# Kernel optimization log

Measured on AMD Instinct MI355X. Metric: run time of the kernel, lower is better.

The kernel has to match this reference:

```python
import jax, jax.numpy as jnp
import numpy as np

V, E, H, L = 32000, 512, 512, 2   # vocab, emb_dim, hidden_dim, lstm layers
IN = 2 * H                        # input_size (= enc_output feature dim)
B, S_ENC, T_DEC = 32, 128, 64


def setup_inputs() -> dict:
    key = jax.random.key(0)
    ks = jax.random.split(key, 20)
    sc = 0.05
    inp = {
        "tokens": jax.random.randint(ks[0], (B, T_DEC), 0, V),
        "enc_output": jax.random.normal(ks[1], (B, S_ENC, IN), jnp.float32),
        "enc_h": jax.random.normal(ks[2], (L, B, H), jnp.float32),
        "enc_c": jax.random.normal(ks[3], (L, B, H), jnp.float32),
        "emb": jax.random.normal(ks[4], (V, E), jnp.float32) * sc,
        # attention MLP: attn1 in = H*L + IN, out = 4H; attn2: 4H -> 1
        "attn1_w": jax.random.normal(ks[5], (4 * H, H * L + IN), jnp.float32) * sc,
        "attn1_b": jnp.zeros((4 * H,), jnp.float32),
        "attn2_w": jax.random.normal(ks[6], (1, 4 * H), jnp.float32) * sc,
        "attn2_b": jnp.zeros((1,), jnp.float32),
        # LSTM layer 0: input E + IN; layer 1: input H. PyTorch gate order i,f,g,o
        "w_ih0": jax.random.normal(ks[7], (4 * H, E + IN), jnp.float32) * sc,
        "w_hh0": jax.random.normal(ks[8], (4 * H, H), jnp.float32) * sc,
        "b_ih0": jnp.zeros((4 * H,), jnp.float32),
        "b_hh0": jnp.zeros((4 * H,), jnp.float32),
        "w_ih1": jax.random.normal(ks[9], (4 * H, H), jnp.float32) * sc,
        "w_hh1": jax.random.normal(ks[10], (4 * H, H), jnp.float32) * sc,
        "b_ih1": jnp.zeros((4 * H,), jnp.float32),
        "b_hh1": jnp.zeros((4 * H,), jnp.float32),
        "out_w": jax.random.normal(ks[11], (V, H), jnp.float32) * sc,
        "out_b": jnp.zeros((V,), jnp.float32),
    }
    return inp


def _lstm_cell(x, h, c, w_ih, w_hh, b_ih, b_hh):
    g = x @ w_ih.T + h @ w_hh.T + (b_ih + b_hh)
    i, f, gg, o = jnp.split(g, 4, axis=-1)
    c_new = jax.nn.sigmoid(f) * c + jax.nn.sigmoid(i) * jnp.tanh(gg)
    h_new = jax.nn.sigmoid(o) * jnp.tanh(c_new)
    return h_new, c_new


def reference(tokens, enc_output, enc_h, enc_c, emb,
              attn1_w, attn1_b, attn2_w, attn2_b,
              w_ih0, w_hh0, b_ih0, b_hh0,
              w_ih1, w_hh1, b_ih1, b_hh1,
              out_w, out_b):
    b, s_enc = enc_output.shape[0], enc_output.shape[1]

    def context(h):  # h: [L, B, H] -> context: [B, 2H]
        hflat = jnp.transpose(h, (1, 0, 2)).reshape(b, -1)          # [B, L*H]
        hexp = jnp.broadcast_to(hflat[:, None, :], (b, s_enc, hflat.shape[-1]))
        ai = jnp.concatenate([enc_output, hexp], axis=-1)           # [B, S, 2H+L*H]
        hid = ai @ attn1_w.T + attn1_b                               # [B, S, 4H]
        logits = hid @ attn2_w.T + attn2_b                           # [B, S, 1]
        w = jax.nn.softmax(logits, axis=1)
        return jnp.sum(enc_output * w, axis=1)                       # [B, 2H]

    def step(carry, emb_t):  # emb_t: [B, E]
        h, c = carry
        ctx = context(h)
        x = jnp.concatenate([emb_t, ctx], axis=-1)                   # [B, E+2H]
        h0, c0 = _lstm_cell(x, h[0], c[0], w_ih0, w_hh0, b_ih0, b_hh0)
        h1, c1 = _lstm_cell(h0, h[1], c[1], w_ih1, w_hh1, b_ih1, b_hh1)
        return (jnp.stack([h0, h1]), jnp.stack([c0, c1])), h1

    emb_seq = jnp.transpose(emb[tokens], (1, 0, 2))                  # [T, B, E]
    _, outs = jax.lax.scan(step, (enc_h, enc_c), emb_seq)            # [T, B, H]
    dec = jnp.transpose(outs, (1, 0, 2))                             # [B, T, H]
    return dec @ out_w.T + out_b                                     # [B, T, V]
```

## Files before the change

kernel.cpp:

```cpp
#include <hip/hip_runtime.h>
#include <hip/hip_bf16.h>

typedef __attribute__((ext_vector_type(4))) float f4v;
typedef __attribute__((ext_vector_type(4))) short s4v;
typedef __attribute__((ext_vector_type(8))) short s8v;

#define DEVINL __device__ __forceinline__
#define NBLK 128
#define PADK 536
#define WROWS (16 * PADK)
#define HSLOT 16384

DEVINL short f2bf(float f) {
  unsigned u = __float_as_uint(f);
  u += 0x7FFFu + ((u >> 16) & 1u);
  return (short)(u >> 16);
}
DEVINL float bf2f(short s) {
  return __uint_as_float(((unsigned)(unsigned short)s) << 16);
}
DEVINL float sigm(float x) { return 1.f / (1.f + expf(-x)); }

DEVINL void cstore64(short* p, unsigned long long d) {
  asm volatile("global_store_dwordx2 %0, %1, off sc0 sc1"
               :: "v"(p), "v"(d) : "memory");
}

__global__ __launch_bounds__(256) void k_init2(const float* __restrict__ enc_h,
                                               short* __restrict__ hbuf,
                                               unsigned* __restrict__ arr) {
  int i = blockIdx.x * 256 + threadIdx.x;
  hbuf[i] = f2bf(enc_h[i]);
  hbuf[(long)65 * HSLOT + i] = f2bf(enc_h[16384 + i]);
  if (i < NBLK * 32 + 32) arr[i] = 0u;
}

__global__ __launch_bounds__(256) void k_weff(const float* __restrict__ attn1_w,
                                              const float* __restrict__ attn2_w,
                                              float* __restrict__ w_enc) {
  __shared__ float part[8][32];
  int t = threadIdx.x;
  int jl = t & 31, kp = t >> 5;
  int j = blockIdx.x * 32 + jl;
  float acc = 0.f;
  for (int k = kp * 256; k < kp * 256 + 256; ++k)
    acc += attn2_w[k] * attn1_w[(long)k * 2048 + j];
  part[kp][jl] = acc;
  __syncthreads();
  if (t < 32) {
    float s = 0.f;
    for (int p = 0; p < 8; ++p) s += part[p][t];
    w_enc[blockIdx.x * 32 + t] = s;
  }
}

__global__ __launch_bounds__(256) void k_attn(const float* __restrict__ enc,
                                              const float* __restrict__ w_enc,
                                              float* __restrict__ ctx) {
  __shared__ float red[256];
  __shared__ float wls[128];
  int b = blockIdx.x, t = threadIdx.x;
  int s = t >> 1, half = t & 1;
  const float* e = enc + ((long)b * 128 + s) * 1024 + half * 512;
  const float* wv = w_enc + half * 512;
  float acc = 0.f;
  for (int k = 0; k < 512; k += 4) {
    f4v ev = *(const f4v*)(e + k);
    f4v w4 = *(const f4v*)(wv + k);
    acc += ev[0] * w4[0] + ev[1] * w4[1] + ev[2] * w4[2] + ev[3] * w4[3];
  }
  red[t] = acc;
  __syncthreads();
  if (half == 0) wls[s] = red[t] + red[t + 1];
  __syncthreads();
  red[t] = (t < 128) ? wls[t] : -3.4e38f;
  __syncthreads();
  for (int off = 128; off >= 1; off >>= 1) {
    if (t < off) red[t] = fmaxf(red[t], red[t + off]);
    __syncthreads();
  }
  float mx = red[0];
  __syncthreads();
  if (t < 128) { float ex = expf(wls[t] - mx); wls[t] = ex; red[t] = ex; }
  else red[t] = 0.f;
  __syncthreads();
  for (int off = 128; off >= 1; off >>= 1) {
    if (t < off) red[t] += red[t + off];
    __syncthreads();
  }
  float inv = 1.f / red[0];
  __syncthreads();
  if (t < 128) wls[t] *= inv;
  __syncthreads();
  float a0 = 0.f, a1 = 0.f, a2 = 0.f, a3 = 0.f;
  for (int ss = 0; ss < 128; ++ss) {
    float w = wls[ss];
    const float* er = enc + ((long)b * 128 + ss) * 1024;
    a0 += w * er[t];
    a1 += w * er[t + 256];
    a2 += w * er[t + 512];
    a3 += w * er[t + 768];
  }
  ctx[b * 1024 + t] = a0;
  ctx[b * 1024 + t + 256] = a1;
  ctx[b * 1024 + t + 512] = a2;
  ctx[b * 1024 + t + 768] = a3;
}

__global__ __launch_bounds__(256) void k_ctxpre(const float* __restrict__ w_ih0,
                                                const float* __restrict__ b_ih0,
                                                const float* __restrict__ b_hh0,
                                                const float* __restrict__ ctx,
                                                float* __restrict__ ctxpre) {
  int t = threadIdx.x;
  int j = blockIdx.x * 8 + (t >> 5);
  int b = t & 31;
  float acc = b_ih0[j] + b_hh0[j];
  const float* w = w_ih0 + (long)j * 1536 + 512;
  const float* c = ctx + b * 1024;
  for (int k = 0; k < 1024; k += 4) {
    f4v wv = *(const f4v*)(w + k);
    f4v cv = *(const f4v*)(c + k);
    acc += wv[0] * cv[0] + wv[1] * cv[1] + wv[2] * cv[2] + wv[3] * cv[3];
  }
  ctxpre[b * 2048 + j] = acc;
}

__global__ __launch_bounds__(256) void k_cvt(const float* __restrict__ src,
                                             short* __restrict__ dst) {
  long i = ((long)blockIdx.x * 256 + threadIdx.x) * 8;
  f4v a = *(const f4v*)(src + i);
  f4v b = *(const f4v*)(src + i + 4);
  s8v o;
  o[0] = f2bf(a[0]); o[1] = f2bf(a[1]); o[2] = f2bf(a[2]); o[3] = f2bf(a[3]);
  o[4] = f2bf(b[0]); o[5] = f2bf(b[1]); o[6] = f2bf(b[2]); o[7] = f2bf(b[3]);
  *(s8v*)(dst + i) = o;
}

template <int MODE>
__global__ __launch_bounds__(256) void gemm_bf16(
    const float* __restrict__ A, const float* __restrict__ B,
    const int* __restrict__ a_rows, const float* __restrict__ bias,
    float* __restrict__ C, int K, int lda, int ldb, int ldc) {
  __shared__ short As[128 * 72];
  __shared__ short Bs[128 * 72];
  int n0 = blockIdx.x * 128, m0 = blockIdx.y * 128;
  int t = threadIdx.x;
  int lane = t & 63, w = t >> 6;
  int wm = w & 1, wn = w >> 1;
  f4v acc[4][4];
#pragma unroll
  for (int mi = 0; mi < 4; ++mi)
#pragma unroll
    for (int ni = 0; ni < 4; ++ni) acc[mi][ni] = (f4v){0.f, 0.f, 0.f, 0.f};

  int sr = t >> 1;
  int sh = (t & 1) * 32;
  long arow = a_rows ? (long)a_rows[m0 + sr] : (long)(m0 + sr);
  const float* ap = A + arow * lda + sh;
  const float* bp = B + (long)(n0 + sr) * ldb + sh;
  short* as = &As[sr * 72 + sh];
  short* bs = &Bs[sr * 72 + sh];

  for (int k0 = 0; k0 < K; k0 += 64) {
#pragma unroll
    for (int i = 0; i < 8; ++i) {
      f4v va = *(const f4v*)(ap + k0 + i * 4);
      f4v vb = *(const f4v*)(bp + k0 + i * 4);
      s4v sa, sb;
      sa[0] = f2bf(va[0]); sa[1] = f2bf(va[1]); sa[2] = f2bf(va[2]); sa[3] = f2bf(va[3]);
      sb[0] = f2bf(vb[0]); sb[1] = f2bf(vb[1]); sb[2] = f2bf(vb[2]); sb[3] = f2bf(vb[3]);
      *(s4v*)(as + i * 4) = sa;
      *(s4v*)(bs + i * 4) = sb;
    }
    __syncthreads();
#pragma unroll
    for (int ks = 0; ks < 2; ++ks) {
      s8v af[4], bf[4];
#pragma unroll
      for (int mi = 0; mi < 4; ++mi)
        af[mi] = *(const s8v*)&As[(wm * 64 + mi * 16 + (lane & 15)) * 72 + ks * 32 + (lane >> 4) * 8];
#pragma unroll
      for (int ni = 0; ni < 4; ++ni)
        bf[ni] = *(const s8v*)&Bs[(wn * 64 + ni * 16 + (lane & 15)) * 72 + ks * 32 + (lane >> 4) * 8];
#pragma unroll
      for (int mi = 0; mi < 4; ++mi)
#pragma unroll
        for (int ni = 0; ni < 4; ++ni)
          acc[mi][ni] = __builtin_amdgcn_mfma_f32_16x16x32_bf16(af[mi], bf[ni], acc[mi][ni], 0, 0, 0);
    }
    __syncthreads();
  }
  int fq = lane >> 4, fr = lane & 15;
#pragma unroll
  for (int mi = 0; mi < 4; ++mi)
#pragma unroll
    for (int ni = 0; ni < 4; ++ni) {
      int col = n0 + wn * 64 + ni * 16 + fr;
      long rowb = m0 + wm * 64 + mi * 16 + fq * 4;
      if (MODE == 2) {
        int bz = (col & 511) >> 2;
        int c = ((col >> 9) << 2) + (col & 3);
#pragma unroll
        for (int r = 0; r < 4; ++r) {
          long m = rowb + r;
          C[(long)bz * 32768 + (m & 63) * 512 + (m >> 6) * 16 + c] = acc[mi][ni][r];
        }
      } else {
        float bv = bias ? bias[col] : 0.f;
#pragma unroll
        for (int r = 0; r < 4; ++r) C[(rowb + r) * (long)ldc + col] = acc[mi][ni][r] + bv;
      }
    }
}

template <bool BCVT>
__global__ __launch_bounds__(256) void gemm_out(
    const short* __restrict__ A, const short* __restrict__ Bbf,
    const float* __restrict__ Bf, const float* __restrict__ bias,
    float* __restrict__ C) {
  __shared__ short As[128 * 72];
  __shared__ short Bs[128 * 72];
  int m0 = blockIdx.x * 128, n0 = blockIdx.y * 128;
  int t = threadIdx.x;
  int lane = t & 63, w = t >> 6;
  int wm = w & 1, wn = w >> 1;
  f4v acc[4][4];
#pragma unroll
  for (int mi = 0; mi < 4; ++mi)
#pragma unroll
    for (int ni = 0; ni < 4; ++ni) acc[mi][ni] = (f4v){0.f, 0.f, 0.f, 0.f};

  int sr = t >> 1;
  int sh = (t & 1) * 32;
  const short* ap = A + (long)(m0 + sr) * 512 + sh;
  const short* bpb = Bbf + (long)(n0 + sr) * 512 + sh;
  const float* bpf = Bf + (long)(n0 + sr) * 512 + sh;
  short* as = &As[sr * 72 + sh];
  short* bs = &Bs[sr * 72 + sh];

  for (int k0 = 0; k0 < 512; k0 += 64) {
#pragma unroll
    for (int i = 0; i < 4; ++i)
      *(s8v*)(as + i * 8) = *(const s8v*)(ap + k0 + i * 8);
    if (BCVT) {
#pragma unroll
      for (int i = 0; i < 8; ++i) {
        f4v vb = *(const f4v*)(bpf + k0 + i * 4);
        s4v sb;
        sb[0] = f2bf(vb[0]); sb[1] = f2bf(vb[1]); sb[2] = f2bf(vb[2]); sb[3] = f2bf(vb[3]);
        *(s4v*)(bs + i * 4) = sb;
      }
    } else {
#pragma unroll
      for (int i = 0; i < 4; ++i)
        *(s8v*)(bs + i * 8) = *(const s8v*)(bpb + k0 + i * 8);
    }
    __syncthreads();
#pragma unroll
    for (int ks = 0; ks < 2; ++ks) {
      s8v af[4], bf[4];
#pragma unroll
      for (int mi = 0; mi < 4; ++mi)
        af[mi] = *(const s8v*)&As[(wm * 64 + mi * 16 + (lane & 15)) * 72 + ks * 32 + (lane >> 4) * 8];
#pragma unroll
      for (int ni = 0; ni < 4; ++ni)
        bf[ni] = *(const s8v*)&Bs[(wn * 64 + ni * 16 + (lane & 15)) * 72 + ks * 32 + (lane >> 4) * 8];
#pragma unroll
      for (int mi = 0; mi < 4; ++mi)
#pragma unroll
        for (int ni = 0; ni < 4; ++ni)
          acc[mi][ni] = __builtin_amdgcn_mfma_f32_16x16x32_bf16(af[mi], bf[ni], acc[mi][ni], 0, 0, 0);
    }
    __syncthreads();
  }
  int fq = lane >> 4, fr = lane & 15;
#pragma unroll
  for (int mi = 0; mi < 4; ++mi)
#pragma unroll
    for (int ni = 0; ni < 4; ++ni) {
      int col = n0 + wn * 64 + ni * 16 + fr;
      float bv = bias[col];
      long rowb = m0 + wm * 64 + mi * 16 + fq * 4;
#pragma unroll
      for (int r = 0; r < 4; ++r)
        __builtin_nontemporal_store(acc[mi][ni][r] + bv, &C[(rowb + r) * 32000L + col]);
    }
}

__global__ __launch_bounds__(256, 1) void lstm_persist(
    const float* __restrict__ w_hh0, const float* __restrict__ w_ih1,
    const float* __restrict__ w_hh1,
    const float* __restrict__ b_ih1, const float* __restrict__ b_hh1,
    const float* __restrict__ enc_c,
    const float* __restrict__ embp2, const float* __restrict__ ctxpre,
    short* __restrict__ hbuf, short* __restrict__ h1seqbf,
    unsigned* __restrict__ arr) {
  __shared__ alignas(16) short wlds[6 * WROWS];
  __shared__ float ctxp_l[32][16];
  __shared__ float bias1_l[16];
  __shared__ float gbuf[2][32][17];

  const int tid = threadIdx.x;
  const bool is_l0 = (blockIdx.x < NBLK);
  const int bz = is_l0 ? blockIdx.x : blockIdx.x - NBLK;
  const int hb4 = bz * 4;
  const int lane = tid & 63, wid = tid >> 6;
  const int mt = wid & 1, kh = wid >> 1;
  const int fr = lane & 15, fq = lane >> 4;

  const int nmat = is_l0 ? 1 : 2;
  for (int base = tid * 4; base < nmat * 16 * 512; base += 1024) {
    int row = base >> 9, k = base & 511;
    int m = row >> 4, c = row & 15;
    int j = ((c >> 2) << 9) + hb4 + (c & 3);
    const float* wsrc = is_l0 ? w_hh0 : (m == 0 ? w_ih1 : w_hh1);
    f4v v = *(const f4v*)(wsrc + (long)j * 512 + k);
    short* hi = &wlds[(m * 2) * WROWS + c * PADK + k];
    short* lo = &wlds[(m * 2 + 1) * WROWS + c * PADK + k];
#pragma unroll
    for (int e = 0; e < 4; ++e) {
      short hh = f2bf(v[e]);
      hi[e] = hh;
      lo[e] = f2bf(v[e] - bf2f(hh));
    }
  }
  if (is_l0) {
    for (int i = tid; i < 512; i += 256) {
      int b = i >> 4, c = i & 15;
      ctxp_l[b][c] = ctxpre[b * 2048 + ((c >> 2) << 9) + hb4 + (c & 3)];
    }
  } else if (tid < 16) {
    int j = ((tid >> 2) << 9) + hb4 + (tid & 3);
    bias1_l[tid] = b_ih1[j] + b_hh1[j];
  }
  const int cq = (tid & 127) >> 2, cr = tid & 3;
  float cst = 0.f;
  if (tid < 128)
    cst = enc_c[(is_l0 ? 0 : 16384) + cq * 512 + hb4 + cr];
  __syncthreads();
  asm volatile("s_waitcnt vmcnt(0)" ::: "memory");
  asm volatile("buffer_inv sc1" ::: "memory");
  __syncthreads();

  short* H0 = hbuf;
  short* H1 = hbuf + (long)65 * HSLOT;
  const int foff = (mt * 16 + fr) * 512 + kh * 256 + fq * 8;
  const int woff = fr * PADK + kh * 256 + fq * 8;

  if (is_l0) {
    for (int p = 0; p < 64; ++p) {
      float e4[4];
      if (tid < 128) {
        const float* ep = embp2 + (long)bz * 32768 + p * 512 + cq * 16 + cr;
#pragma unroll
        for (int g = 0; g < 4; ++g) e4[g] = ep[g * 4];
      }
      if (p) {
        if (tid < NBLK)
          while (__hip_atomic_load(&arr[tid << 5], __ATOMIC_RELAXED,
                                   __HIP_MEMORY_SCOPE_AGENT) < (unsigned)p)
            __builtin_amdgcn_s_sleep(1);
        __syncthreads();
      }
      const short* a0 = H0 + (long)p * HSLOT + foff;
      f4v l0h = {0.f, 0.f, 0.f, 0.f}, l0l = l0h;
      const short* b0h = &wlds[0 * WROWS + woff];
      const short* b0l = &wlds[1 * WROWS + woff];
#pragma unroll
      for (int ks = 0; ks < 8; ++ks) {
        s8v A0 = *(const s8v*)(a0 + ks * 32);
        s8v B0h = *(const s8v*)(b0h + ks * 32);
        s8v B0l = *(const s8v*)(b0l + ks * 32);
        l0h = __builtin_amdgcn_mfma_f32_16x16x32_bf16(A0, B0h, l0h, 0, 0, 0);
        l0l = __builtin_amdgcn_mfma_f32_16x16x32_bf16(A0, B0l, l0l, 0, 0, 0);
      }
      f4v s = l0h + l0l;
#pragma unroll
      for (int r = 0; r < 4; ++r) gbuf[kh][mt * 16 + fq * 4 + r][fr] = s[r];
      __syncthreads();
      if (tid < 128) {
        float g4[4];
#pragma unroll
        for (int g = 0; g < 4; ++g) {
          int c = g * 4 + cr;
          g4[g] = gbuf[0][cq][c] + gbuf[1][cq][c] + ctxp_l[cq][c] + e4[g];
        }
        float cn = sigm(g4[1]) * cst + sigm(g4[0]) * tanhf(g4[2]);
        float hn = sigm(g4[3]) * tanhf(cn);
        cst = cn;
        unsigned v16 = (unsigned)(unsigned short)f2bf(hn);
        unsigned p01 = v16 | ((unsigned)__shfl_down((int)v16, 1) << 16);
        unsigned long long wd = (unsigned long long)p01 |
            ((unsigned long long)(unsigned)__shfl_down((int)p01, 2) << 32);
        if ((tid & 3) == 0)
          cstore64(H0 + (long)(p + 1) * HSLOT + cq * 512 + hb4, wd);
      }
      asm volatile("s_waitcnt vmcnt(0)" ::: "memory");
      __syncthreads();
      if (tid == 0)
        __hip_atomic_store(&arr[(unsigned)bz << 5], (unsigned)(p + 1),
                           __ATOMIC_RELAXED, __HIP_MEMORY_SCOPE_AGENT);
    }
  } else {
    for (int p = 1; p <= 64; ++p) {
      if (tid < NBLK)
        while (__hip_atomic_load(&arr[tid << 5], __ATOMIC_RELAXED,
                                 __HIP_MEMORY_SCOPE_AGENT) < (unsigned)p)
          __builtin_amdgcn_s_sleep(2);
      __syncthreads();
      const short* a0 = H0 + (long)p * HSLOT + foff;
      f4v x1h = {0.f, 0.f, 0.f, 0.f}, x1l = x1h, h1h = x1h, h1l = x1h;
      const short* b2h = &wlds[0 * WROWS + woff];
      const short* b2l = &wlds[1 * WROWS + woff];
#pragma unroll
      for (int ks = 0; ks < 8; ++ks) {
        s8v A0 = *(const s8v*)(a0 + ks * 32);
        s8v B2h = *(const s8v*)(b2h + ks * 32);
        s8v B2l = *(const s8v*)(b2l + ks * 32);
        x1h = __builtin_amdgcn_mfma_f32_16x16x32_bf16(A0, B2h, x1h, 0, 0, 0);
        x1l = __builtin_amdgcn_mfma_f32_16x16x32_bf16(A0, B2l, x1l, 0, 0, 0);
      }
      if (p > 1) {
        if (tid < NBLK)
          while (__hip_atomic_load(&arr[(tid << 5) + 16], __ATOMIC_RELAXED,
                                   __HIP_MEMORY_SCOPE_AGENT) < (unsigned)(p - 1))
            __builtin_amdgcn_s_sleep(2);
        __syncthreads();
      }
      const short* a1 = H1 + (long)(p - 1) * HSLOT + foff;
      const short* b4h = &wlds[2 * WROWS + woff];
      const short* b4l = &wlds[3 * WROWS + woff];
#pragma unroll
      for (int ks = 0; ks < 8; ++ks) {
        s8v A1 = *(const s8v*)(a1 + ks * 32);
        s8v B4h = *(const s8v*)(b4h + ks * 32);
        s8v B4l = *(const s8v*)(b4l + ks * 32);
        h1h = __builtin_amdgcn_mfma_f32_16x16x32_bf16(A1, B4h, h1h, 0, 0, 0);
        h1l = __builtin_amdgcn_mfma_f32_16x16x32_bf16(A1, B4l, h1l, 0, 0, 0);
      }
      f4v s = x1h + x1l + h1h + h1l;
#pragma unroll
      for (int r = 0; r < 4; ++r) gbuf[kh][mt * 16 + fq * 4 + r][fr] = s[r];
      __syncthreads();
      if (tid < 128) {
        float g4[4];
#pragma unroll
        for (int g = 0; g < 4; ++g) {
          int c = g * 4 + cr;
          g4[g] = gbuf[0][cq][c] + gbuf[1][cq][c] + bias1_l[c];
        }
        float cn = sigm(g4[1]) * cst + sigm(g4[0]) * tanhf(g4[2]);
        float hn = sigm(g4[3]) * tanhf(cn);
        cst = cn;
        unsigned v16 = (unsigned)(unsigned short)f2bf(hn);
        unsigned p01 = v16 | ((unsigned)__shfl_down((int)v16, 1) << 16);
        unsigned long long wd = (unsigned long long)p01 |
            ((unsigned long long)(unsigned)__shfl_down((int)p01, 2) << 32);
        if ((tid & 3) == 0) {
          if (p < 64)
            cstore64(H1 + (long)p * HSLOT + cq * 512 + hb4, wd);
          *(unsigned long long*)&h1seqbf[((long)cq * 64 + (p - 1)) * 512 + hb4] = wd;
        }
      }
      if (p < 64) {
        asm volatile("s_waitcnt vmcnt(0)" ::: "memory");
        __syncthreads();
        if (tid == 0)
          __hip_atomic_store(&arr[((unsigned)bz << 5) + 16], (unsigned)p,
                             __ATOMIC_RELAXED, __HIP_MEMORY_SCOPE_AGENT);
      }
    }
  }
}

extern "C" void kernel_launch(void* const* d_in, const int* in_sizes, int n_in,
                              void* d_out, int out_size, void* d_ws, size_t ws_size,
                              hipStream_t stream) {
  const int*   tokens  = (const int*)  d_in[0];
  const float* enc_out = (const float*)d_in[1];
  const float* enc_h   = (const float*)d_in[2];
  const float* enc_c   = (const float*)d_in[3];
  const float* emb     = (const float*)d_in[4];
  const float* attn1_w = (const float*)d_in[5];
  const float* attn2_w = (const float*)d_in[7];
  const float* w_ih0   = (const float*)d_in[9];
  const float* w_hh0   = (const float*)d_in[10];
  const float* b_ih0   = (const float*)d_in[11];
  const float* b_hh0   = (const float*)d_in[12];
  const float* w_ih1   = (const float*)d_in[13];
  const float* w_hh1   = (const float*)d_in[14];
  const float* b_ih1   = (const float*)d_in[15];
  const float* b_hh1   = (const float*)d_in[16];
  const float* out_w   = (const float*)d_in[17];
  const float* out_b   = (const float*)d_in[18];
  float* out = (float*)d_out;

  float* f = (float*)d_ws;
  float*    w_enc    = f;
  float*    ctx      = f + 1024;
  float*    ctxpre   = f + 33792;
  float*    embp2    = f + 99328;
  short*    h1seqbf  = (short*)(f + 4293632);
  short*    hbuf     = (short*)(f + 4817920);
  unsigned* arr      = (unsigned*)(f + 5882880);
  short*    out_w_bf = (short*)(f + 5887040);
  const size_t NEED = (size_t)(5887040 + 8192000) * 4;
  const bool big = ws_size >= NEED;

  k_init2<<<64, 256, 0, stream>>>(enc_h, hbuf, arr);
  k_weff<<<32, 256, 0, stream>>>(attn1_w, attn2_w, w_enc);
  k_attn<<<32, 256, 0, stream>>>(enc_out, w_enc, ctx);
  k_ctxpre<<<256, 256, 0, stream>>>(w_ih0, b_ih0, b_hh0, ctx, ctxpre);
  gemm_bf16<2><<<dim3(16, 16), 256, 0, stream>>>(emb, w_ih0, tokens, nullptr,
                                                 embp2, 512, 512, 1536, 0);
  if (big) k_cvt<<<8000, 256, 0, stream>>>(out_w, out_w_bf);
  lstm_persist<<<2 * NBLK, 256, 0, stream>>>(w_hh0, w_ih1, w_hh1, b_ih1, b_hh1,
                                             enc_c, embp2, ctxpre, hbuf,
                                             h1seqbf, arr);
  if (big)
    gemm_out<false><<<dim3(16, 250), 256, 0, stream>>>(h1seqbf, out_w_bf, nullptr,
                                                       out_b, out);
  else
    gemm_out<true><<<dim3(16, 250), 256, 0, stream>>>(h1seqbf, nullptr, out_w,
                                                      out_b, out);
}
```

Measured before the change: 556.1 us.

## Shrink persistent LSTM blocks to two waves, dropping K-split reduction

The persistent LSTM kernel now runs 128 threads per block instead of 256. Each wave owns 16 batch rows and the full K=512 reduction, rather than splitting K across two waves and summing partial gates through shared memory. All threads now take part in the gate nonlinearity and the spin-wait polling. The intent is to cut per-step cross-wave reduction and idle threads on the serial recurrence critical path, at the cost of twice as many MFMA steps per wave.

```diff
diff --git a/kernel.cpp b/kernel.cpp
--- a/kernel.cpp
+++ b/kernel.cpp
@@ -288,7 +288,7 @@
     }
 }
 
-__global__ __launch_bounds__(256, 1) void lstm_persist(
+__global__ __launch_bounds__(128, 1) void lstm_persist(
     const float* __restrict__ w_hh0, const float* __restrict__ w_ih1,
     const float* __restrict__ w_hh1,
     const float* __restrict__ b_ih1, const float* __restrict__ b_hh1,
@@ -297,20 +297,19 @@
     short* __restrict__ hbuf, short* __restrict__ h1seqbf,
     unsigned* __restrict__ arr) {
   __shared__ alignas(16) short wlds[6 * WROWS];
-  __shared__ float ctxp_l[32][16];
+  __shared__ float ctxp_l[32][17];
   __shared__ float bias1_l[16];
-  __shared__ float gbuf[2][32][17];
+  __shared__ float gw[2][16][17];
 
   const int tid = threadIdx.x;
   const bool is_l0 = (blockIdx.x < NBLK);
   const int bz = is_l0 ? blockIdx.x : blockIdx.x - NBLK;
   const int hb4 = bz * 4;
-  const int lane = tid & 63, wid = tid >> 6;
-  const int mt = wid & 1, kh = wid >> 1;
+  const int lane = tid & 63, w = tid >> 6;
   const int fr = lane & 15, fq = lane >> 4;
 
   const int nmat = is_l0 ? 1 : 2;
-  for (int base = tid * 4; base < nmat * 16 * 512; base += 1024) {
+  for (int base = tid * 4; base < nmat * 16 * 512; base += 512) {
     int row = base >> 9, k = base & 511;
     int m = row >> 4, c = row & 15;
     int j = ((c >> 2) << 9) + hb4 + (c & 3);
@@ -326,18 +325,16 @@
     }
   }
   if (is_l0) {
-    for (int i = tid; i < 512; i += 256) {
-      int b = i >> 4, c = i & 15;
-      ctxp_l[b][c] = ctxpre[b * 2048 + ((c >> 2) << 9) + hb4 + (c & 3)];
-    }
+    for (int i = tid; i < 512; i += 128)
+      ctxp_l[i >> 4][i & 15] =
+          ctxpre[(i >> 4) * 2048 + (((i & 15) >> 2) << 9) + hb4 + (i & 3)];
   } else if (tid < 16) {
     int j = ((tid >> 2) << 9) + hb4 + (tid & 3);
     bias1_l[tid] = b_ih1[j] + b_hh1[j];
   }
-  const int cq = (tid & 127) >> 2, cr = tid & 3;
-  float cst = 0.f;
-  if (tid < 128)
-    cst = enc_c[(is_l0 ? 0 : 16384) + cq * 512 + hb4 + cr];
+  const int rr = (tid & 63) >> 2, d = tid & 3;
+  const int batch = w * 16 + rr;
+  float cst = enc_c[(is_l0 ? 0 : 16384) + batch * 512 + hb4 + d];
   __syncthreads();
   asm volatile("s_waitcnt vmcnt(0)" ::: "memory");
   asm volatile("buffer_inv sc1" ::: "memory");
@@ -345,57 +342,57 @@
 
   short* H0 = hbuf;
   short* H1 = hbuf + (long)65 * HSLOT;
-  const int foff = (mt * 16 + fr) * 512 + kh * 256 + fq * 8;
-  const int woff = fr * PADK + kh * 256 + fq * 8;
+  const int foff = (w * 16 + fr) * 512 + fq * 8;
+  const int woff = fr * PADK + fq * 8;
 
   if (is_l0) {
     for (int p = 0; p < 64; ++p) {
       float e4[4];
-      if (tid < 128) {
-        const float* ep = embp2 + (long)bz * 32768 + p * 512 + cq * 16 + cr;
+      {
+        const float* ep = embp2 + (long)bz * 32768 + p * 512 + batch * 16 + d;
 #pragma unroll
         for (int g = 0; g < 4; ++g) e4[g] = ep[g * 4];
       }
       if (p) {
-        if (tid < NBLK)
-          while (__hip_atomic_load(&arr[tid << 5], __ATOMIC_RELAXED,
-                                   __HIP_MEMORY_SCOPE_AGENT) < (unsigned)p)
-            __builtin_amdgcn_s_sleep(1);
+        while (__hip_atomic_load(&arr[tid << 5], __ATOMIC_RELAXED,
+                                 __HIP_MEMORY_SCOPE_AGENT) < (unsigned)p)
+          __builtin_amdgcn_s_sleep(1);
         __syncthreads();
       }
       const short* a0 = H0 + (long)p * HSLOT + foff;
-      f4v l0h = {0.f, 0.f, 0.f, 0.f}, l0l = l0h;
       const short* b0h = &wlds[0 * WROWS + woff];
       const short* b0l = &wlds[1 * WROWS + woff];
-#pragma unroll
-      for (int ks = 0; ks < 8; ++ks) {
+      f4v h0a = {0.f, 0.f, 0.f, 0.f}, h1a = h0a, l0a = h0a, l1a = h0a;
+#pragma unroll
+      for (int ks = 0; ks < 16; ks += 2) {
         s8v A0 = *(const s8v*)(a0 + ks * 32);
+        s8v A1 = *(const s8v*)(a0 + ks * 32 + 32);
         s8v B0h = *(const s8v*)(b0h + ks * 32);
+        s8v B1h = *(const s8v*)(b0h + ks * 32 + 32);
         s8v B0l = *(const s8v*)(b0l + ks * 32);
-        l0h = __builtin_amdgcn_mfma_f32_16x16x32_bf16(A0, B0h, l0h, 0, 0, 0);
-        l0l = __builtin_amdgcn_mfma_f32_16x16x32_bf16(A0, B0l, l0l, 0, 0, 0);
-      }
-      f4v s = l0h + l0l;
-#pragma unroll
-      for (int r = 0; r < 4; ++r) gbuf[kh][mt * 16 + fq * 4 + r][fr] = s[r];
+        s8v B1l = *(const s8v*)(b0l + ks * 32 + 32);
+        h0a = __builtin_amdgcn_mfma_f32_16x16x32_bf16(A0, B0h, h0a, 0, 0, 0);
+        l0a = __builtin_amdgcn_mfma_f32_16x16x32_bf16(A0, B0l, l0a, 0, 0, 0);
+        h1a = __builtin_amdgcn_mfma_f32_16x16x32_bf16(A1, B1h, h1a, 0, 0, 0);
+        l1a = __builtin_amdgcn_mfma_f32_16x16x32_bf16(A1, B1l, l1a, 0, 0, 0);
+      }
+      f4v s = h0a + h1a + l0a + l1a;
+#pragma unroll
+      for (int r = 0; r < 4; ++r) gw[w][fq * 4 + r][fr] = s[r];
       __syncthreads();
-      if (tid < 128) {
-        float g4[4];
-#pragma unroll
-        for (int g = 0; g < 4; ++g) {
-          int c = g * 4 + cr;
-          g4[g] = gbuf[0][cq][c] + gbuf[1][cq][c] + ctxp_l[cq][c] + e4[g];
-        }
-        float cn = sigm(g4[1]) * cst + sigm(g4[0]) * tanhf(g4[2]);
-        float hn = sigm(g4[3]) * tanhf(cn);
-        cst = cn;
-        unsigned v16 = (unsigned)(unsigned short)f2bf(hn);
-        unsigned p01 = v16 | ((unsigned)__shfl_down((int)v16, 1) << 16);
-        unsigned long long wd = (unsigned long long)p01 |
-            ((unsigned long long)(unsigned)__shfl_down((int)p01, 2) << 32);
-        if ((tid & 3) == 0)
-          cstore64(H0 + (long)(p + 1) * HSLOT + cq * 512 + hb4, wd);
-      }
+      float g4[4];
+#pragma unroll
+      for (int g = 0; g < 4; ++g)
+        g4[g] = gw[w][rr][g * 4 + d] + ctxp_l[batch][g * 4 + d] + e4[g];
+      float cn = sigm(g4[1]) * cst + sigm(g4[0]) * tanhf(g4[2]);
+      float hn = sigm(g4[3]) * tanhf(cn);
+      cst = cn;
+      unsigned v16 = (unsigned)(unsigned short)f2bf(hn);
+      unsigned p01 = v16 | ((unsigned)__shfl_down((int)v16, 1) << 16);
+      unsigned long long wd = (unsigned long long)p01 |
+          ((unsigned long long)(unsigned)__shfl_down((int)p01, 2) << 32);
+      if ((tid & 3) == 0)
+        cstore64(H0 + (long)(p + 1) * HSLOT + batch * 512 + hb4, wd);
       asm volatile("s_waitcnt vmcnt(0)" ::: "memory");
       __syncthreads();
       if (tid == 0)
@@ -404,64 +401,58 @@
     }
   } else {
     for (int p = 1; p <= 64; ++p) {
-      if (tid < NBLK)
-        while (__hip_atomic_load(&arr[tid << 5], __ATOMIC_RELAXED,
-                                 __HIP_MEMORY_SCOPE_AGENT) < (unsigned)p)
-          __builtin_amdgcn_s_sleep(2);
+      while (__hip_atomic_load(&arr[tid << 5], __ATOMIC_RELAXED,
+                               __HIP_MEMORY_SCOPE_AGENT) < (unsigned)p)
+        __builtin_amdgcn_s_sleep(2);
       __syncthreads();
       const short* a0 = H0 + (long)p * HSLOT + foff;
-      f4v x1h = {0.f, 0.f, 0.f, 0.f}, x1l = x1h, h1h = x1h, h1l = x1h;
       const short* b2h = &wlds[0 * WROWS + woff];
       const short* b2l = &wlds[1 * WROWS + woff];
-#pragma unroll
-      for (int ks = 0; ks < 8; ++ks) {
+      f4v xh = {0.f, 0.f, 0.f, 0.f}, xl = xh, hh = xh, hl = xh;
+#pragma unroll
+      for (int ks = 0; ks < 16; ++ks) {
         s8v A0 = *(const s8v*)(a0 + ks * 32);
         s8v B2h = *(const s8v*)(b2h + ks * 32);
         s8v B2l = *(const s8v*)(b2l + ks * 32);
-        x1h = __builtin_amdgcn_mfma_f32_16x16x32_bf16(A0, B2h, x1h, 0, 0, 0);
-        x1l = __builtin_amdgcn_mfma_f32_16x16x32_bf16(A0, B2l, x1l, 0, 0, 0);
+        xh = __builtin_amdgcn_mfma_f32_16x16x32_bf16(A0, B2h, xh, 0, 0, 0);
+        xl = __builtin_amdgcn_mfma_f32_16x16x32_bf16(A0, B2l, xl, 0, 0, 0);
       }
       if (p > 1) {
-        if (tid < NBLK)
-          while (__hip_atomic_load(&arr[(tid << 5) + 16], __ATOMIC_RELAXED,
-                                   __HIP_MEMORY_SCOPE_AGENT) < (unsigned)(p - 1))
-            __builtin_amdgcn_s_sleep(2);
+        while (__hip_atomic_load(&arr[(tid << 5) + 16], __ATOMIC_RELAXED,
+                                 __HIP_MEMORY_SCOPE_AGENT) < (unsigned)(p - 1))
+          __builtin_amdgcn_s_sleep(2);
         __syncthreads();
       }
       const short* a1 = H1 + (long)(p - 1) * HSLOT + foff;
       const short* b4h = &wlds[2 * WROWS + woff];
       const short* b4l = &wlds[3 * WROWS + woff];
 #pragma unroll
-      for (int ks = 0; ks < 8; ++ks) {
+      for (int ks = 0; ks < 16; ++ks) {
         s8v A1 = *(const s8v*)(a1 + ks * 32);
         s8v B4h = *(const s8v*)(b4h + ks * 32);
         s8v B4l = *(const s8v*)(b4l + ks * 32);
-        h1h = __builtin_amdgcn_mfma_f32_16x16x32_bf16(A1, B4h, h1h, 0, 0, 0);
-        h1l = __builtin_amdgcn_mfma_f32_16x16x32_bf16(A1, B4l, h1l, 0, 0, 0);
-      }
-      f4v s = x1h + x1l + h1h + h1l;
-#pragma unroll
-      for (int r = 0; r < 4; ++r) gbuf[kh][mt * 16 + fq * 4 + r][fr] = s[r];
+        hh = __builtin_amdgcn_mfma_f32_16x16x32_bf16(A1, B4h, hh, 0, 0, 0);
+        hl = __builtin_amdgcn_mfma_f32_16x16x32_bf16(A1, B4l, hl, 0, 0, 0);
+      }
+      f4v s = xh + xl + hh + hl;
+#pragma unroll
+      for (int r = 0; r < 4; ++r) gw[w][fq * 4 + r][fr] = s[r];
       __syncthreads();
-      if (tid < 128) {
-        float g4[4];
-#pragma unroll
-        for (int g = 0; g < 4; ++g) {
-          int c = g * 4 + cr;
-          g4[g] = gbuf[0][cq][c] + gbuf[1][cq][c] + bias1_l[c];
-        }
-        float cn = sigm(g4[1]) * cst + sigm(g4[0]) * tanhf(g4[2]);
-        float hn = sigm(g4[3]) * tanhf(cn);
-        cst = cn;
-        unsigned v16 = (unsigned)(unsigned short)f2bf(hn);
-        unsigned p01 = v16 | ((unsigned)__shfl_down((int)v16, 1) << 16);
-        unsigned long long wd = (unsigned long long)p01 |
-            ((unsigned long long)(unsigned)__shfl_down((int)p01, 2) << 32);
-        if ((tid & 3) == 0) {
-          if (p < 64)
-            cstore64(H1 + (long)p * HSLOT + cq * 512 + hb4, wd);
-          *(unsigned long long*)&h1seqbf[((long)cq * 64 + (p - 1)) * 512 + hb4] = wd;
-        }
+      float g4[4];
+#pragma unroll
+      for (int g = 0; g < 4; ++g)
+        g4[g] = gw[w][rr][g * 4 + d] + bias1_l[g * 4 + d];
+      float cn = sigm(g4[1]) * cst + sigm(g4[0]) * tanhf(g4[2]);
+      float hn = sigm(g4[3]) * tanhf(cn);
+      cst = cn;
+      unsigned v16 = (unsigned)(unsigned short)f2bf(hn);
+      unsigned p01 = v16 | ((unsigned)__shfl_down((int)v16, 1) << 16);
+      unsigned long long wd = (unsigned long long)p01 |
+          ((unsigned long long)(unsigned)__shfl_down((int)p01, 2) << 32);
+      if ((tid & 3) == 0) {
+        if (p < 64)
+          cstore64(H1 + (long)p * HSLOT + batch * 512 + hb4, wd);
+        *(unsigned long long*)&h1seqbf[((long)batch * 64 + (p - 1)) * 512 + hb4] = wd;
       }
       if (p < 64) {
         asm volatile("s_waitcnt vmcnt(0)" ::: "memory");
@@ -515,7 +506,7 @@
   gemm_bf16<2><<<dim3(16, 16), 256, 0, stream>>>(emb, w_ih0, tokens, nullptr,
                                                  embp2, 512, 512, 1536, 0);
   if (big) k_cvt<<<8000, 256, 0, stream>>>(out_w, out_w_bf);
-  lstm_persist<<<2 * NBLK, 256, 0, stream>>>(w_hh0, w_ih1, w_hh1, b_ih1, b_hh1,
+  lstm_persist<<<2 * NBLK, 128, 0, stream>>>(w_hh0, w_ih1, w_hh1, b_ih1, b_hh1,
                                              enc_c, embp2, ctxpre, hbuf,
                                              h1seqbf, arr);
   if (big)
```

After: 649.8 us. +16.8%, slower.

## Split attention into parallel logit and context kernels; convert output weights inline

Applied to the files above, without the earlier changes.

The single 32-block attention kernel is split into two launches. One computes logits across 256 blocks; the other does the softmax and builds the weighted context across 128 blocks, each covering a quarter of the feature dimension. This is meant to remove the low-parallelism bottleneck of the old attention pass. The separate fp32-to-bf16 conversion pass over the output weight matrix is also removed, and the output GEMM now always converts the weights while loading its tiles. That avoids a 65 MB read/write pass, at the cost of redundant conversion work across the 16 row tiles.

```diff
diff --git a/kernel.cpp b/kernel.cpp
--- a/kernel.cpp
+++ b/kernel.cpp
@@ -54,26 +54,40 @@
   }
 }
 
-__global__ __launch_bounds__(256) void k_attn(const float* __restrict__ enc,
-                                              const float* __restrict__ w_enc,
-                                              float* __restrict__ ctx) {
-  __shared__ float red[256];
-  __shared__ float wls[128];
-  int b = blockIdx.x, t = threadIdx.x;
-  int s = t >> 1, half = t & 1;
-  const float* e = enc + ((long)b * 128 + s) * 1024 + half * 512;
-  const float* wv = w_enc + half * 512;
+__global__ __launch_bounds__(256) void k_attn_lg(const float* __restrict__ enc,
+                                                 const float* __restrict__ w_enc,
+                                                 float* __restrict__ logits) {
+  __shared__ float red[16][17];
+  int b = blockIdx.x >> 3, sp = blockIdx.x & 7;
+  int t = threadIdx.x, row = t >> 4, kc = t & 15;
+  int s = sp * 16 + row;
+  const float* e = enc + ((long)b * 128 + s) * 1024 + kc * 64;
+  const float* wv = w_enc + kc * 64;
   float acc = 0.f;
-  for (int k = 0; k < 512; k += 4) {
+  for (int k = 0; k < 64; k += 4) {
     f4v ev = *(const f4v*)(e + k);
     f4v w4 = *(const f4v*)(wv + k);
     acc += ev[0] * w4[0] + ev[1] * w4[1] + ev[2] * w4[2] + ev[3] * w4[3];
   }
-  red[t] = acc;
-  __syncthreads();
-  if (half == 0) wls[s] = red[t] + red[t + 1];
-  __syncthreads();
-  red[t] = (t < 128) ? wls[t] : -3.4e38f;
+  red[row][kc] = acc;
+  __syncthreads();
+  if (kc == 0) {
+    float sm = 0.f;
+#pragma unroll
+    for (int i = 0; i < 16; ++i) sm += red[row][i];
+    logits[b * 128 + s] = sm;
+  }
+}
+
+__global__ __launch_bounds__(256) void k_attn_cx(const float* __restrict__ enc,
+                                                 const float* __restrict__ logits,
+                                                 float* __restrict__ ctx) {
+  __shared__ float wls[128];
+  __shared__ float red[256];
+  int b = blockIdx.x >> 2, ch = blockIdx.x & 3;
+  int t = threadIdx.x;
+  float lv = (t < 128) ? logits[b * 128 + t] : -3.4e38f;
+  red[t] = lv;
   __syncthreads();
   for (int off = 128; off >= 1; off >>= 1) {
     if (t < off) red[t] = fmaxf(red[t], red[t + off]);
@@ -81,30 +95,21 @@
   }
   float mx = red[0];
   __syncthreads();
-  if (t < 128) { float ex = expf(wls[t] - mx); wls[t] = ex; red[t] = ex; }
-  else red[t] = 0.f;
+  float ex = 0.f;
+  if (t < 128) { ex = expf(lv - mx); wls[t] = ex; }
+  red[t] = ex;
   __syncthreads();
   for (int off = 128; off >= 1; off >>= 1) {
     if (t < off) red[t] += red[t + off];
     __syncthreads();
   }
   float inv = 1.f / red[0];
-  __syncthreads();
-  if (t < 128) wls[t] *= inv;
-  __syncthreads();
-  float a0 = 0.f, a1 = 0.f, a2 = 0.f, a3 = 0.f;
-  for (int ss = 0; ss < 128; ++ss) {
-    float w = wls[ss];
-    const float* er = enc + ((long)b * 128 + ss) * 1024;
-    a0 += w * er[t];
-    a1 += w * er[t + 256];
-    a2 += w * er[t + 512];
-    a3 += w * er[t + 768];
-  }
-  ctx[b * 1024 + t] = a0;
-  ctx[b * 1024 + t + 256] = a1;
-  ctx[b * 1024 + t + 512] = a2;
-  ctx[b * 1024 + t + 768] = a3;
+  int dim = ch * 256 + t;
+  const float* eb = enc + (long)b * 131072 + dim;
+  float a = 0.f;
+#pragma unroll 4
+  for (int ss = 0; ss < 128; ++ss) a += wls[ss] * eb[ss * 1024];
+  ctx[b * 1024 + dim] = a * inv;
 }
 
 __global__ __launch_bounds__(256) void k_ctxpre(const float* __restrict__ w_ih0,
@@ -126,17 +131,6 @@
   ctxpre[b * 2048 + j] = acc;
 }
 
-__global__ __launch_bounds__(256) void k_cvt(const float* __restrict__ src,
-                                             short* __restrict__ dst) {
-  long i = ((long)blockIdx.x * 256 + threadIdx.x) * 8;
-  f4v a = *(const f4v*)(src + i);
-  f4v b = *(const f4v*)(src + i + 4);
-  s8v o;
-  o[0] = f2bf(a[0]); o[1] = f2bf(a[1]); o[2] = f2bf(a[2]); o[3] = f2bf(a[3]);
-  o[4] = f2bf(b[0]); o[5] = f2bf(b[1]); o[6] = f2bf(b[2]); o[7] = f2bf(b[3]);
-  *(s8v*)(dst + i) = o;
-}
-
 template <int MODE>
 __global__ __launch_bounds__(256) void gemm_bf16(
     const float* __restrict__ A, const float* __restrict__ B,
@@ -214,11 +208,9 @@
     }
 }
 
-template <bool BCVT>
 __global__ __launch_bounds__(256) void gemm_out(
-    const short* __restrict__ A, const short* __restrict__ Bbf,
-    const float* __restrict__ Bf, const float* __restrict__ bias,
-    float* __restrict__ C) {
+    const short* __restrict__ A, const float* __restrict__ Bf,
+    const float* __restrict__ bias, float* __restrict__ C) {
   __shared__ short As[128 * 72];
   __shared__ short Bs[128 * 72];
   int m0 = blockIdx.x * 128, n0 = blockIdx.y * 128;
@@ -234,7 +226,6 @@
   int sr = t >> 1;
   int sh = (t & 1) * 32;
   const short* ap = A + (long)(m0 + sr) * 512 + sh;
-  const short* bpb = Bbf + (long)(n0 + sr) * 512 + sh;
   const float* bpf = Bf + (long)(n0 + sr) * 512 + sh;
   short* as = &As[sr * 72 + sh];
   short* bs = &Bs[sr * 72 + sh];
@@ -243,18 +234,12 @@
 #pragma unroll
     for (int i = 0; i < 4; ++i)
       *(s8v*)(as + i * 8) = *(const s8v*)(ap + k0 + i * 8);
-    if (BCVT) {
-#pragma unroll
-      for (int i = 0; i < 8; ++i) {
-        f4v vb = *(const f4v*)(bpf + k0 + i * 4);
-        s4v sb;
-        sb[0] = f2bf(vb[0]); sb[1] = f2bf(vb[1]); sb[2] = f2bf(vb[2]); sb[3] = f2bf(vb[3]);
-        *(s4v*)(bs + i * 4) = sb;
-      }
-    } else {
-#pragma unroll
-      for (int i = 0; i < 4; ++i)
-        *(s8v*)(bs + i * 8) = *(const s8v*)(bpb + k0 + i * 8);
+#pragma unroll
+    for (int i = 0; i < 8; ++i) {
+      f4v vb = *(const f4v*)(bpf + k0 + i * 4);
+      s4v sb;
+      sb[0] = f2bf(vb[0]); sb[1] = f2bf(vb[1]); sb[2] = f2bf(vb[2]); sb[3] = f2bf(vb[3]);
+      *(s4v*)(bs + i * 4) = sb;
     }
     __syncthreads();
 #pragma unroll
@@ -504,24 +489,17 @@
   short*    h1seqbf  = (short*)(f + 4293632);
   short*    hbuf     = (short*)(f + 4817920);
   unsigned* arr      = (unsigned*)(f + 5882880);
-  short*    out_w_bf = (short*)(f + 5887040);
-  const size_t NEED = (size_t)(5887040 + 8192000) * 4;
-  const bool big = ws_size >= NEED;
+  float*    logits   = f + 5887040;
 
   k_init2<<<64, 256, 0, stream>>>(enc_h, hbuf, arr);
   k_weff<<<32, 256, 0, stream>>>(attn1_w, attn2_w, w_enc);
-  k_attn<<<32, 256, 0, stream>>>(enc_out, w_enc, ctx);
+  k_attn_lg<<<256, 256, 0, stream>>>(enc_out, w_enc, logits);
+  k_attn_cx<<<128, 256, 0, stream>>>(enc_out, logits, ctx);
   k_ctxpre<<<256, 256, 0, stream>>>(w_ih0, b_ih0, b_hh0, ctx, ctxpre);
   gemm_bf16<2><<<dim3(16, 16), 256, 0, stream>>>(emb, w_ih0, tokens, nullptr,
                                                  embp2, 512, 512, 1536, 0);
-  if (big) k_cvt<<<8000, 256, 0, stream>>>(out_w, out_w_bf);
   lstm_persist<<<2 * NBLK, 256, 0, stream>>>(w_hh0, w_ih1, w_hh1, b_ih1, b_hh1,
                                              enc_c, embp2, ctxpre, hbuf,
                                              h1seqbf, arr);
-  if (big)
-    gemm_out<false><<<dim3(16, 250), 256, 0, stream>>>(h1seqbf, out_w_bf, nullptr,
-                                                       out_b, out);
-  else
-    gemm_out<true><<<dim3(16, 250), 256, 0, stream>>>(h1seqbf, nullptr, out_w,
-                                                      out_b, out);
-}
+  gemm_out<<<dim3(16, 250), 256, 0, stream>>>(h1seqbf, out_w, out_b, out);
+}
```

New measurement: 597.5 us. 1.07x slower.
